# Kernel optimization log

Hardware: AMD Instinct MI355X
Metric: run time of the kernel (lower is better)

## Reference

```python
import jax, jax.numpy as jnp
import numpy as np

B, CIN, COUT, N, M, K = 8, 128, 256, 8192, 2048, 16
BN_EPS = 1e-5


def setup_inputs() -> dict:
    key = jax.random.key(0)
    k1, k2, k3 = jax.random.split(key, 3)
    x = jax.random.normal(k1, (B, CIN, N), dtype=jnp.float32)
    coords = jax.random.normal(k2, (B, 3, N), dtype=jnp.float32)
    W = jax.random.normal(k3, (COUT, CIN), dtype=jnp.float32) * 0.05  # 1x1 conv, bias=False
    gamma = jnp.ones((COUT,), dtype=jnp.float32)   # BatchNorm2d weight
    beta = jnp.zeros((COUT,), dtype=jnp.float32)   # BatchNorm2d bias
    return {"x": x, "coords": coords, "W": W, "gamma": gamma, "beta": beta}


def furthest_point_sampling(coords, num_samples):
    """coords: (B,3,N) -> indices (B,num_samples) int32. Greedy FPS starting at index 0."""
    pts = coords.transpose(0, 2, 1)  # (B,N,3)
    b, n, _ = pts.shape
    idx0 = jnp.zeros((b,), dtype=jnp.int32)
    mind0 = jnp.full((b, n), 1e10, dtype=pts.dtype)

    def step(carry, _):
        mind, last = carry
        lastpt = jnp.take_along_axis(pts, last[:, None, None], axis=1)  # (b,1,3)
        d = jnp.sum((pts - lastpt) ** 2, axis=-1)                        # (b,n)
        mind = jnp.minimum(mind, d)
        nxt = jnp.argmax(mind, axis=-1).astype(jnp.int32)
        return (mind, nxt), nxt

    (_, _), rest = jax.lax.scan(step, (mind0, idx0), None, length=num_samples - 1)
    return jnp.concatenate([idx0[:, None], rest.T], axis=1)  # (b,num_samples)


def reference(x, coords, W, gamma, beta):
    b = x.shape[0]
    fps_idx = furthest_point_sampling(coords, M)                # (B,M)
    pts = coords.transpose(0, 2, 1)                             # (B,N,3)
    bidx = jnp.arange(b)[:, None]
    fps_pts = pts[bidx, fps_idx]                                # (B,M,3)

    # squared-distance matrix via ||a||^2 + ||b||^2 - 2ab (avoids (B,M,N,3) temp)
    d = (jnp.sum(fps_pts ** 2, -1)[:, :, None]
         + jnp.sum(pts ** 2, -1)[:, None, :]
         - 2.0 * jnp.einsum('bmd,bnd->bmn', fps_pts, pts))      # (B,M,N)
    _, knn_idx = jax.lax.top_k(-d, K)                           # (B,M,K) nearest (sorted)

    x_t = x.transpose(0, 2, 1)                                  # (B,N,Cin)
    knn = x_t[jnp.arange(b)[:, None, None], knn_idx]            # (B,M,K,Cin)

    # PointwiseConv2D: 1x1 conv (no bias) + BatchNorm2d (batch stats) + ReLU
    h = jnp.einsum('bmkc,oc->bmko', knn, W)                     # (B,M,K,Cout)
    mean = jnp.mean(h, axis=(0, 1, 2))
    var = jnp.var(h, axis=(0, 1, 2))
    h = (h - mean) * jax.lax.rsqrt(var + BN_EPS) * gamma + beta
    h = jax.nn.relu(h)

    y = jnp.max(h, axis=2).transpose(0, 2, 1)                   # (B,Cout,M), max over k
    fps_coords = fps_pts.transpose(0, 2, 1)                     # (B,3,M)
    return y, fps_coords
```

## Files before the change

### kernel.cpp

```cpp
#include <hip/hip_runtime.h>
#include <math.h>

#define B_ 8
#define CIN_ 128
#define COUT_ 256
#define N_ 8192
#define M_ 2048
#define K_ 16

#define GEMM_BLOCKS 2048

__device__ __forceinline__ unsigned umax2(unsigned a, unsigned b) { return a > b ? a : b; }
__device__ __forceinline__ unsigned umin2(unsigned a, unsigned b) { return a < b ? a : b; }

__device__ __forceinline__ unsigned wave_reduce_umax(unsigned v) {
    v = umax2(v, (unsigned)__builtin_amdgcn_update_dpp(0, (int)v, 0x111, 0xf, 0xf, false));
    v = umax2(v, (unsigned)__builtin_amdgcn_update_dpp(0, (int)v, 0x112, 0xf, 0xf, false));
    v = umax2(v, (unsigned)__builtin_amdgcn_update_dpp(0, (int)v, 0x114, 0xf, 0xf, false));
    v = umax2(v, (unsigned)__builtin_amdgcn_update_dpp(0, (int)v, 0x118, 0xf, 0xf, false));
    v = umax2(v, (unsigned)__builtin_amdgcn_update_dpp(0, (int)v, 0x142, 0xf, 0xf, false));
    v = umax2(v, (unsigned)__builtin_amdgcn_update_dpp(0, (int)v, 0x143, 0xf, 0xf, false));
    return (unsigned)__builtin_amdgcn_readlane((int)v, 63);
}
__device__ __forceinline__ unsigned wave_reduce_umin(unsigned v) {
    v = umin2(v, (unsigned)__builtin_amdgcn_update_dpp(-1, (int)v, 0x111, 0xf, 0xf, false));
    v = umin2(v, (unsigned)__builtin_amdgcn_update_dpp(-1, (int)v, 0x112, 0xf, 0xf, false));
    v = umin2(v, (unsigned)__builtin_amdgcn_update_dpp(-1, (int)v, 0x114, 0xf, 0xf, false));
    v = umin2(v, (unsigned)__builtin_amdgcn_update_dpp(-1, (int)v, 0x118, 0xf, 0xf, false));
    v = umin2(v, (unsigned)__builtin_amdgcn_update_dpp(-1, (int)v, 0x142, 0xf, 0xf, false));
    v = umin2(v, (unsigned)__builtin_amdgcn_update_dpp(-1, (int)v, 0x143, 0xf, 0xf, false));
    return (unsigned)__builtin_amdgcn_readlane((int)v, 63);
}

__global__ __launch_bounds__(512) void fps_gemm_kernel(const float* __restrict__ coords,
                                                       const float* __restrict__ x,
                                                       const float* __restrict__ W,
                                                       float* __restrict__ fpts,
                                                       float* __restrict__ out_fps,
                                                       float* __restrict__ hp,
                                                       int* __restrict__ counts) {
    __shared__ union {
        struct {
            float4 pts[N_];
            unsigned long long kbuf[2][8];
            int wlist[M_];
        } f;
        struct {
            float Xs[64][128];
            float Wt[64][68];
        } g;
    } sm;

    const int tid = threadIdx.x;

    if (blockIdx.x < B_) {
#pragma clang fp contract(off)
        const int b = blockIdx.x;
        const int lane = tid & 63;
        const int wid = tid >> 6;
        const float* cb = coords + (size_t)b * 3 * N_;
        float4* pts = sm.f.pts;
        unsigned long long (*kbuf)[8] = sm.f.kbuf;
        int* wlist = sm.f.wlist;

        float px[16], py[16], pz[16], mind[16];
#pragma unroll
        for (int s = 0; s < 16; ++s) {
            int p = tid + s * 512;
            px[s] = cb[p];
            py[s] = cb[N_ + p];
            pz[s] = cb[2 * N_ + p];
            mind[s] = 1e10f;
            pts[p] = make_float4(px[s], py[s], pz[s], 0.f);
        }
        __syncthreads();
        float4 p0 = pts[0];
        float lx = p0.x, ly = p0.y, lz = p0.z;

        int par = 0;
        for (int m = 1; m < M_; ++m) {
            float bv = -1.0f; int bs = 0;
#pragma unroll
            for (int s = 0; s < 16; ++s) {
                float dx = px[s] - lx;
                float dy = py[s] - ly;
                float dz = pz[s] - lz;
                float d = __builtin_fmaf(dz, dz, __builtin_fmaf(dy, dy, dx * dx));
                float mn = fminf(mind[s], d);
                mind[s] = mn;
                if (mn > bv) { bv = mn; bs = s; }
            }
            int bi = tid + bs * 512;
            unsigned kd = __float_as_uint(bv);
            unsigned md = wave_reduce_umax(kd);
            unsigned cand = (kd == md) ? (unsigned)bi : 0xffffffffu;
            unsigned mi = wave_reduce_umin(cand);
            if (lane == 0)
                kbuf[par][wid] = ((unsigned long long)md << 32) |
                                 (unsigned long long)(0xffffffffu - mi);
            __syncthreads();
            const unsigned long long* kb = kbuf[par];
            ulonglong2 q0 = *(const ulonglong2*)&kb[0];
            ulonglong2 q1 = *(const ulonglong2*)&kb[2];
            ulonglong2 q2 = *(const ulonglong2*)&kb[4];
            ulonglong2 q3 = *(const ulonglong2*)&kb[6];
            unsigned long long a0 = q0.x > q0.y ? q0.x : q0.y;
            unsigned long long a1 = q1.x > q1.y ? q1.x : q1.y;
            unsigned long long a2 = q2.x > q2.y ? q2.x : q2.y;
            unsigned long long a3 = q3.x > q3.y ? q3.x : q3.y;
            unsigned long long b01 = a0 > a1 ? a0 : a1;
            unsigned long long b23 = a2 > a3 ? a2 : a3;
            unsigned long long best = b01 > b23 ? b01 : b23;
            int widx = (int)(0xffffffffu - (unsigned)(best & 0xffffffffull));
            widx = ((unsigned)widx < (unsigned)N_) ? widx : 0;
            float4 wp = pts[widx];
            lx = wp.x; ly = wp.y; lz = wp.z;
            if (tid == 0) wlist[m] = widx;
            par ^= 1;
        }

        __syncthreads();
        for (int mm = tid; mm < M_; mm += 512) {
            int wi = (mm == 0) ? 0 : wlist[mm];
            wi = ((unsigned)wi < (unsigned)N_) ? wi : 0;
            float4 wp = pts[wi];
            ((float4*)fpts)[b * M_ + mm] = make_float4(wp.x, wp.y, wp.z, 0.f);
            out_fps[(size_t)b * 3 * M_ + 0 * M_ + mm] = wp.x;
            out_fps[(size_t)b * 3 * M_ + 1 * M_ + mm] = wp.y;
            out_fps[(size_t)b * 3 * M_ + 2 * M_ + mm] = wp.z;
        }
    } else {
        const int gb = blockIdx.x - B_;
        if (tid < 32) counts[gb * 32 + tid] = 0;

        const int b = gb >> 8;
        const int rem = gb & 255;
        const int n0 = (rem >> 2) * 128;
        const int o0 = (rem & 3) * 64;
        const int tn = (tid & 31) * 4;
        const int to = (tid >> 5) * 4;
        const float* xg = x + (size_t)b * CIN_ * N_;
        float (*Xs)[128] = sm.g.Xs;
        float (*Wt)[68] = sm.g.Wt;

        float acc[4][4] = {};
        for (int kk = 0; kk < CIN_; kk += 64) {
#pragma unroll
            for (int i = 0; i < 16; ++i) {
                int e = tid + 512 * i;
                int r = e >> 7, q = e & 127;
                Xs[r][q] = xg[(size_t)(kk + r) * N_ + n0 + q];
            }
#pragma unroll
            for (int i = 0; i < 8; ++i) {
                int e = tid + 512 * i;
                int r = e >> 6, q = e & 63;
                Wt[q][r] = W[(size_t)(o0 + r) * CIN_ + kk + q];
            }
            __syncthreads();
#pragma unroll 8
            for (int c = 0; c < 64; ++c) {
                float4 a = *(const float4*)&Xs[c][tn];
                float4 bb = *(const float4*)&Wt[c][to];
                float av[4] = {a.x, a.y, a.z, a.w};
                float bv[4] = {bb.x, bb.y, bb.z, bb.w};
#pragma unroll
                for (int j = 0; j < 4; ++j)
#pragma unroll
                    for (int l = 0; l < 4; ++l)
                        acc[j][l] += av[j] * bv[l];
            }
            __syncthreads();
        }
#pragma unroll
        for (int j = 0; j < 4; ++j) {
            float4 v = make_float4(acc[j][0], acc[j][1], acc[j][2], acc[j][3]);
            *(float4*)&hp[((size_t)b * N_ + n0 + tn + j) * COUT_ + o0 + to] = v;
        }
    }
}

__global__ __launch_bounds__(256) void knn_kernel(const float* __restrict__ coords,
                                                  const float* __restrict__ fpts,
                                                  int* __restrict__ knn,
                                                  int* __restrict__ counts) {
#pragma clang fp contract(off)
    const int bidx = blockIdx.x;
    const int b = bidx >> 9;
    const int mg = bidx & 511;
    const int tid = threadIdx.x;
    const int lane = tid & 63;
    const int w = tid >> 6;
    const int m = mg * 4 + w;
    const int row = b * M_ + m;
    const float* cb = coords + (size_t)b * 3 * N_;

    __shared__ float4 tile[1024];

    float4 f = ((const float4*)fpts)[row];
    const float fx = f.x, fy = f.y, fz = f.z;
    const float sf = __builtin_fmaf(fz, fz, __builtin_fmaf(fy, fy, fx * fx));

    float ed = INFINITY; int ei = 0x7fffffff;
    float tau_d = INFINITY; int tau_i = 0x7fffffff;

    for (int t = 0; t < 8; ++t) {
        const int base = t * 1024;
#pragma unroll
        for (int j = 0; j < 4; ++j) {
            int idx = tid + 256 * j;
            int n = base + idx;
            float gx = cb[n], gy = cb[N_ + n], gz = cb[2 * N_ + n];
            float sp = __builtin_fmaf(gz, gz, __builtin_fmaf(gy, gy, gx * gx));
            tile[idx] = make_float4(gx, gy, gz, sp);
        }
        __syncthreads();
        for (int s = 0; s < 16; ++s) {
            int l = s * 64 + lane;
            float4 p = tile[l];
            int n = base + l;
            float dot = __builtin_fmaf(fz, p.z, __builtin_fmaf(fy, p.y, fx * p.x));
            float d = (sf + p.w) - 2.0f * dot;
            bool q = (d < tau_d) || (d == tau_d && n < tau_i);
            unsigned long long bal = __ballot(q);
            while (bal) {
                int lb = __ffsll(bal) - 1;
                bal &= bal - 1;
                float dv = __shfl(d, lb);
                int   iv = __shfl(n, lb);
                if ((dv < tau_d) || (dv == tau_d && iv < tau_i)) {
                    float pud = __shfl_up(ed, 1);
                    int   pui = __shfl_up(ei, 1);
                    bool cs = (dv < ed) || (dv == ed && iv < ei);
                    bool cp = (lane != 0) && ((dv < pud) || (dv == pud && iv < pui));
                    ed = cs ? (cp ? pud : dv) : ed;
                    ei = cs ? (cp ? pui : iv) : ei;
                    tau_d = __shfl(ed, 15);
                    tau_i = __shfl(ei, 15);
                }
            }
        }
        __syncthreads();
    }
    if (lane < K_) {
        int v = ei;
        v = ((unsigned)v < (unsigned)N_) ? v : 0;
        knn[(size_t)row * K_ + lane] = v;
        atomicAdd(&counts[b * N_ + v], 1);
    }
}

__global__ __launch_bounds__(256) void stats_partial_kernel(const float* __restrict__ hp,
                                                            const int* __restrict__ counts,
                                                            double* __restrict__ partial,
                                                            double* __restrict__ partial2) {
    const int o = threadIdx.x;
    const int base = blockIdx.x * 256;
    double s = 0.0, s2 = 0.0;
    for (int r = 0; r < 256; ++r) {
        int g = base + r;
        int cnt = counts[g];
        if (cnt) {
            double h = (double)hp[(size_t)g * COUT_ + o];
            double c = (double)cnt;
            double ch = c * h;
            s += ch;
            s2 += ch * h;
        }
    }
    partial[(size_t)blockIdx.x * 256 + o] = s;
    partial2[(size_t)blockIdx.x * 256 + o] = s2;
}

__global__ void bn_final_kernel(const double* __restrict__ partial,
                                const double* __restrict__ partial2,
                                const float* __restrict__ gamma,
                                const float* __restrict__ beta,
                                float* __restrict__ scale,
                                float* __restrict__ bias) {
    int o = threadIdx.x;
    double s = 0.0, s2 = 0.0;
    for (int j = 0; j < 256; ++j) {
        s += partial[(size_t)j * 256 + o];
        s2 += partial2[(size_t)j * 256 + o];
    }
    const double inv = 1.0 / (double)(B_ * M_ * K_);
    double mean = s * inv;
    double var = s2 * inv - mean * mean;
    if (var < 0.0) var = 0.0;
    double r = 1.0 / sqrt(var + 1e-5);
    double g = (double)gamma[o];
    scale[o] = (float)(r * g);
    bias[o] = (float)((double)beta[o] - mean * r * g);
}

__global__ __launch_bounds__(256) void finalize_kernel(const float* __restrict__ hp,
                                                       const int* __restrict__ knn,
                                                       const float* __restrict__ scale,
                                                       const float* __restrict__ bias,
                                                       float* __restrict__ y) {
    const int b = blockIdx.x >> 6;
    const int m0 = (blockIdx.x & 63) * 32;
    const int tid = threadIdx.x;
    __shared__ int kidx[512];
    __shared__ float tile[32][257];

    for (int e = tid; e < 512; e += 256) {
        int n = knn[(b * M_ + m0 + (e >> 4)) * K_ + (e & 15)];
        kidx[e] = ((unsigned)n < (unsigned)N_) ? n : 0;
    }
    __syncthreads();

    const float s = scale[tid];
    const float t = bias[tid];
    const float* hb = hp + (size_t)b * N_ * COUT_;
    for (int mm = 0; mm < 32; ++mm) {
        float v = -INFINITY;
#pragma unroll
        for (int k = 0; k < K_; ++k) {
            int n = kidx[mm * 16 + k];
            float h = hb[(size_t)n * COUT_ + tid];
            v = fmaxf(v, h * s + t);
        }
        v = fmaxf(v, 0.0f);
        tile[mm][tid] = v;
    }
    __syncthreads();
#pragma unroll
    for (int r = 0; r < 32; ++r) {
        int o2 = r * 8 + (tid >> 5);
        int mm = tid & 31;
        y[((size_t)b * COUT_ + o2) * M_ + m0 + mm] = tile[mm][o2];
    }
}

__global__ void sentinel_kernel(float* out, float v) { out[0] = v; }

extern "C" void kernel_launch(void* const* d_in, const int* in_sizes, int n_in,
                              void* d_out, int out_size, void* d_ws, size_t ws_size,
                              hipStream_t stream) {
    const float* x = (const float*)d_in[0];
    const float* coords = (const float*)d_in[1];
    const float* W = (const float*)d_in[2];
    const float* gamma = (const float*)d_in[3];
    const float* beta = (const float*)d_in[4];
    float* y = (float*)d_out;
    float* out_fps = y + (size_t)B_ * COUT_ * M_;

    if (n_in != 5 ||
        in_sizes[0] != B_ * CIN_ * N_ ||
        in_sizes[1] != B_ * 3 * N_ ||
        in_sizes[2] != COUT_ * CIN_ ||
        in_sizes[3] != COUT_ || in_sizes[4] != COUT_ ||
        out_size != B_ * COUT_ * M_ + B_ * 3 * M_) {
        sentinel_kernel<<<1, 1, 0, stream>>>(y, -2.0e6f);
        return;
    }

    const size_t HP_BYTES = (size_t)B_ * N_ * COUT_ * 4;
    const size_t FPTS_BYTES = (size_t)B_ * M_ * 16;
    const size_t KNN_BYTES = (size_t)B_ * M_ * K_ * 4;
    const size_t PART_BYTES = (size_t)256 * 256 * 8;
    const size_t CNT_BYTES = (size_t)B_ * N_ * 4;
    const size_t NEED = HP_BYTES + FPTS_BYTES + KNN_BYTES + 2 * PART_BYTES + CNT_BYTES + 8192;
    if (ws_size < NEED) {
        sentinel_kernel<<<1, 1, 0, stream>>>(y, -1.0e6f);
        return;
    }
    char* ws = (char*)d_ws;
    float* hp = (float*)ws;
    float* fpts = (float*)(ws + HP_BYTES);
    int* knn = (int*)(ws + HP_BYTES + FPTS_BYTES);
    double* partial = (double*)(ws + HP_BYTES + FPTS_BYTES + KNN_BYTES);
    double* partial2 = (double*)(ws + HP_BYTES + FPTS_BYTES + KNN_BYTES + PART_BYTES);
    int* counts = (int*)(ws + HP_BYTES + FPTS_BYTES + KNN_BYTES + 2 * PART_BYTES);
    float* scale = (float*)(ws + HP_BYTES + FPTS_BYTES + KNN_BYTES + 2 * PART_BYTES + CNT_BYTES);
    float* bias = scale + 256;

    fps_gemm_kernel<<<B_ + GEMM_BLOCKS, 512, 0, stream>>>(coords, x, W, fpts, out_fps, hp, counts);
    knn_kernel<<<B_ * 512, 256, 0, stream>>>(coords, fpts, knn, counts);
    stats_partial_kernel<<<256, 256, 0, stream>>>(hp, counts, partial, partial2);
    bn_final_kernel<<<1, 256, 0, stream>>>(partial, partial2, gamma, beta, scale, bias);
    finalize_kernel<<<512, 256, 0, stream>>>(hp, knn, scale, bias, y);
}
```

Baseline: 1.900 ms.

## Fuse FPS, GEMM and KNN into persistent kernel with per-sample flag streaming

Merges the KNN kernel into the FPS+GEMM launch as a persistent kernel with 240 worker blocks. The workers first loop over the GEMM tiles, then spin on per-sample atomic flags that the FPS blocks publish as each point is chosen, so KNN queries overlap with the serial FPS loop instead of waiting for it to finish. This removes the fpts buffer and a kernel launch, and adds two memsets. The risks are spin-wait overhead and a deadlock if not all blocks are co-resident, and the GEMM now runs on fewer blocks.

```diff
diff --git a/kernel.cpp b/kernel.cpp
--- a/kernel.cpp
+++ b/kernel.cpp
@@ -8,7 +8,9 @@
 #define M_ 2048
 #define K_ 16
 
-#define GEMM_BLOCKS 2048
+#define WORKERS 240
+#define NTILE 2048
+#define NGROUP 2048
 
 __device__ __forceinline__ unsigned umax2(unsigned a, unsigned b) { return a > b ? a : b; }
 __device__ __forceinline__ unsigned umin2(unsigned a, unsigned b) { return a < b ? a : b; }
@@ -32,13 +34,14 @@
     return (unsigned)__builtin_amdgcn_readlane((int)v, 63);
 }
 
-__global__ __launch_bounds__(512) void fps_gemm_kernel(const float* __restrict__ coords,
-                                                       const float* __restrict__ x,
-                                                       const float* __restrict__ W,
-                                                       float* __restrict__ fpts,
-                                                       float* __restrict__ out_fps,
-                                                       float* __restrict__ hp,
-                                                       int* __restrict__ counts) {
+__global__ __launch_bounds__(512) void mega_kernel(const float* __restrict__ coords,
+                                                   const float* __restrict__ x,
+                                                   const float* __restrict__ W,
+                                                   unsigned* __restrict__ wflag,
+                                                   float* __restrict__ out_fps,
+                                                   float* __restrict__ hp,
+                                                   int* __restrict__ knn,
+                                                   int* __restrict__ counts) {
     __shared__ union {
         struct {
             float4 pts[N_];
@@ -49,15 +52,18 @@
             float Xs[64][128];
             float Wt[64][68];
         } g;
+        struct {
+            float4 tile[1024];
+        } k;
     } sm;
 
     const int tid = threadIdx.x;
+    const int lane = tid & 63;
+    const int w = tid >> 6;
 
     if (blockIdx.x < B_) {
 #pragma clang fp contract(off)
         const int b = blockIdx.x;
-        const int lane = tid & 63;
-        const int wid = tid >> 6;
         const float* cb = coords + (size_t)b * 3 * N_;
         float4* pts = sm.f.pts;
         unsigned long long (*kbuf)[8] = sm.f.kbuf;
@@ -73,6 +79,9 @@
             mind[s] = 1e10f;
             pts[p] = make_float4(px[s], py[s], pz[s], 0.f);
         }
+        if (tid == 0)
+            __hip_atomic_store(&wflag[(size_t)b * M_], 0u,
+                               __ATOMIC_RELAXED, __HIP_MEMORY_SCOPE_AGENT);
         __syncthreads();
         float4 p0 = pts[0];
         float lx = p0.x, ly = p0.y, lz = p0.z;
@@ -96,8 +105,8 @@
             unsigned cand = (kd == md) ? (unsigned)bi : 0xffffffffu;
             unsigned mi = wave_reduce_umin(cand);
             if (lane == 0)
-                kbuf[par][wid] = ((unsigned long long)md << 32) |
-                                 (unsigned long long)(0xffffffffu - mi);
+                kbuf[par][w] = ((unsigned long long)md << 32) |
+                               (unsigned long long)(0xffffffffu - mi);
             __syncthreads();
             const unsigned long long* kb = kbuf[par];
             ulonglong2 q0 = *(const ulonglong2*)&kb[0];
@@ -115,7 +124,11 @@
             widx = ((unsigned)widx < (unsigned)N_) ? widx : 0;
             float4 wp = pts[widx];
             lx = wp.x; ly = wp.y; lz = wp.z;
-            if (tid == 0) wlist[m] = widx;
+            if (tid == 0) {
+                wlist[m] = widx;
+                __hip_atomic_store(&wflag[(size_t)b * M_ + m], (unsigned)widx,
+                                   __ATOMIC_RELAXED, __HIP_MEMORY_SCOPE_AGENT);
+            }
             par ^= 1;
         }
 
@@ -124,129 +137,130 @@
             int wi = (mm == 0) ? 0 : wlist[mm];
             wi = ((unsigned)wi < (unsigned)N_) ? wi : 0;
             float4 wp = pts[wi];
-            ((float4*)fpts)[b * M_ + mm] = make_float4(wp.x, wp.y, wp.z, 0.f);
             out_fps[(size_t)b * 3 * M_ + 0 * M_ + mm] = wp.x;
             out_fps[(size_t)b * 3 * M_ + 1 * M_ + mm] = wp.y;
             out_fps[(size_t)b * 3 * M_ + 2 * M_ + mm] = wp.z;
         }
     } else {
-        const int gb = blockIdx.x - B_;
-        if (tid < 32) counts[gb * 32 + tid] = 0;
-
-        const int b = gb >> 8;
-        const int rem = gb & 255;
-        const int n0 = (rem >> 2) * 128;
-        const int o0 = (rem & 3) * 64;
-        const int tn = (tid & 31) * 4;
-        const int to = (tid >> 5) * 4;
-        const float* xg = x + (size_t)b * CIN_ * N_;
+        const int wkr = blockIdx.x - B_;
+
         float (*Xs)[128] = sm.g.Xs;
         float (*Wt)[68] = sm.g.Wt;
-
-        float acc[4][4] = {};
-        for (int kk = 0; kk < CIN_; kk += 64) {
-#pragma unroll
-            for (int i = 0; i < 16; ++i) {
-                int e = tid + 512 * i;
-                int r = e >> 7, q = e & 127;
-                Xs[r][q] = xg[(size_t)(kk + r) * N_ + n0 + q];
+        for (int t = wkr; t < NTILE; t += WORKERS) {
+            const int b = t >> 8;
+            const int rem = t & 255;
+            const int n0 = (rem >> 2) * 128;
+            const int o0 = (rem & 3) * 64;
+            const int tn = (tid & 31) * 4;
+            const int to = (tid >> 5) * 4;
+            const float* xg = x + (size_t)b * CIN_ * N_;
+
+            float acc[4][4] = {};
+            for (int kk = 0; kk < CIN_; kk += 64) {
+#pragma unroll
+                for (int i = 0; i < 16; ++i) {
+                    int e = tid + 512 * i;
+                    int r = e >> 7, q = e & 127;
+                    Xs[r][q] = xg[(size_t)(kk + r) * N_ + n0 + q];
+                }
+#pragma unroll
+                for (int i = 0; i < 8; ++i) {
+                    int e = tid + 512 * i;
+                    int r = e >> 6, q = e & 63;
+                    Wt[q][r] = W[(size_t)(o0 + r) * CIN_ + kk + q];
+                }
+                __syncthreads();
+#pragma unroll 8
+                for (int c = 0; c < 64; ++c) {
+                    float4 a = *(const float4*)&Xs[c][tn];
+                    float4 bb = *(const float4*)&Wt[c][to];
+                    float av[4] = {a.x, a.y, a.z, a.w};
+                    float bv[4] = {bb.x, bb.y, bb.z, bb.w};
+#pragma unroll
+                    for (int j = 0; j < 4; ++j)
+#pragma unroll
+                        for (int l = 0; l < 4; ++l)
+                            acc[j][l] += av[j] * bv[l];
+                }
+                __syncthreads();
             }
 #pragma unroll
-            for (int i = 0; i < 8; ++i) {
-                int e = tid + 512 * i;
-                int r = e >> 6, q = e & 63;
-                Wt[q][r] = W[(size_t)(o0 + r) * CIN_ + kk + q];
+            for (int j = 0; j < 4; ++j) {
+                float4 v = make_float4(acc[j][0], acc[j][1], acc[j][2], acc[j][3]);
+                *(float4*)&hp[((size_t)b * N_ + n0 + tn + j) * COUT_ + o0 + to] = v;
             }
-            __syncthreads();
-#pragma unroll 8
-            for (int c = 0; c < 64; ++c) {
-                float4 a = *(const float4*)&Xs[c][tn];
-                float4 bb = *(const float4*)&Wt[c][to];
-                float av[4] = {a.x, a.y, a.z, a.w};
-                float bv[4] = {bb.x, bb.y, bb.z, bb.w};
-#pragma unroll
-                for (int j = 0; j < 4; ++j)
-#pragma unroll
-                    for (int l = 0; l < 4; ++l)
-                        acc[j][l] += av[j] * bv[l];
-            }
-            __syncthreads();
-        }
-#pragma unroll
-        for (int j = 0; j < 4; ++j) {
-            float4 v = make_float4(acc[j][0], acc[j][1], acc[j][2], acc[j][3]);
-            *(float4*)&hp[((size_t)b * N_ + n0 + tn + j) * COUT_ + o0 + to] = v;
-        }
-    }
-}
-
-__global__ __launch_bounds__(256) void knn_kernel(const float* __restrict__ coords,
-                                                  const float* __restrict__ fpts,
-                                                  int* __restrict__ knn,
-                                                  int* __restrict__ counts) {
+        }
+
+        {
 #pragma clang fp contract(off)
-    const int bidx = blockIdx.x;
-    const int b = bidx >> 9;
-    const int mg = bidx & 511;
-    const int tid = threadIdx.x;
-    const int lane = tid & 63;
-    const int w = tid >> 6;
-    const int m = mg * 4 + w;
-    const int row = b * M_ + m;
-    const float* cb = coords + (size_t)b * 3 * N_;
-
-    __shared__ float4 tile[1024];
-
-    float4 f = ((const float4*)fpts)[row];
-    const float fx = f.x, fy = f.y, fz = f.z;
-    const float sf = __builtin_fmaf(fz, fz, __builtin_fmaf(fy, fy, fx * fx));
-
-    float ed = INFINITY; int ei = 0x7fffffff;
-    float tau_d = INFINITY; int tau_i = 0x7fffffff;
-
-    for (int t = 0; t < 8; ++t) {
-        const int base = t * 1024;
-#pragma unroll
-        for (int j = 0; j < 4; ++j) {
-            int idx = tid + 256 * j;
-            int n = base + idx;
-            float gx = cb[n], gy = cb[N_ + n], gz = cb[2 * N_ + n];
-            float sp = __builtin_fmaf(gz, gz, __builtin_fmaf(gy, gy, gx * gx));
-            tile[idx] = make_float4(gx, gy, gz, sp);
-        }
-        __syncthreads();
-        for (int s = 0; s < 16; ++s) {
-            int l = s * 64 + lane;
-            float4 p = tile[l];
-            int n = base + l;
-            float dot = __builtin_fmaf(fz, p.z, __builtin_fmaf(fy, p.y, fx * p.x));
-            float d = (sf + p.w) - 2.0f * dot;
-            bool q = (d < tau_d) || (d == tau_d && n < tau_i);
-            unsigned long long bal = __ballot(q);
-            while (bal) {
-                int lb = __ffsll(bal) - 1;
-                bal &= bal - 1;
-                float dv = __shfl(d, lb);
-                int   iv = __shfl(n, lb);
-                if ((dv < tau_d) || (dv == tau_d && iv < tau_i)) {
-                    float pud = __shfl_up(ed, 1);
-                    int   pui = __shfl_up(ei, 1);
-                    bool cs = (dv < ed) || (dv == ed && iv < ei);
-                    bool cp = (lane != 0) && ((dv < pud) || (dv == pud && iv < pui));
-                    ed = cs ? (cp ? pud : dv) : ed;
-                    ei = cs ? (cp ? pui : iv) : ei;
-                    tau_d = __shfl(ed, 15);
-                    tau_i = __shfl(ei, 15);
+            float4* tile = sm.k.tile;
+            for (int g = wkr; g < NGROUP; g += WORKERS) {
+                const int b = g & 7;
+                const int mg = g >> 3;
+                const int m = mg * 8 + w;
+                const int row = b * M_ + m;
+                const float* cb = coords + (size_t)b * 3 * N_;
+
+                unsigned widx;
+                while ((widx = __hip_atomic_load(&wflag[row], __ATOMIC_RELAXED,
+                                                 __HIP_MEMORY_SCOPE_AGENT)) == 0xffffffffu)
+                    __builtin_amdgcn_s_sleep(2);
+                widx = (widx < (unsigned)N_) ? widx : 0;
+
+                const float fx = cb[widx];
+                const float fy = cb[N_ + widx];
+                const float fz = cb[2 * N_ + widx];
+                const float sf = __builtin_fmaf(fz, fz, __builtin_fmaf(fy, fy, fx * fx));
+
+                float ed = INFINITY; int ei = 0x7fffffff;
+                float tau_d = INFINITY; int tau_i = 0x7fffffff;
+
+                for (int t = 0; t < 8; ++t) {
+                    const int base = t * 1024;
+#pragma unroll
+                    for (int j = 0; j < 2; ++j) {
+                        int idx = tid + 512 * j;
+                        int n = base + idx;
+                        float gx = cb[n], gy = cb[N_ + n], gz = cb[2 * N_ + n];
+                        float sp = __builtin_fmaf(gz, gz, __builtin_fmaf(gy, gy, gx * gx));
+                        tile[idx] = make_float4(gx, gy, gz, sp);
+                    }
+                    __syncthreads();
+                    for (int s = 0; s < 16; ++s) {
+                        int l = s * 64 + lane;
+                        float4 p = tile[l];
+                        int n = base + l;
+                        float dot = __builtin_fmaf(fz, p.z, __builtin_fmaf(fy, p.y, fx * p.x));
+                        float d = (sf + p.w) - 2.0f * dot;
+                        bool q = (d < tau_d) || (d == tau_d && n < tau_i);
+                        unsigned long long bal = __ballot(q);
+                        while (bal) {
+                            int lb = __ffsll(bal) - 1;
+                            bal &= bal - 1;
+                            float dv = __shfl(d, lb);
+                            int   iv = __shfl(n, lb);
+                            if ((dv < tau_d) || (dv == tau_d && iv < tau_i)) {
+                                float pud = __shfl_up(ed, 1);
+                                int   pui = __shfl_up(ei, 1);
+                                bool cs = (dv < ed) || (dv == ed && iv < ei);
+                                bool cp = (lane != 0) && ((dv < pud) || (dv == pud && iv < pui));
+                                ed = cs ? (cp ? pud : dv) : ed;
+                                ei = cs ? (cp ? pui : iv) : ei;
+                                tau_d = __shfl(ed, 15);
+                                tau_i = __shfl(ei, 15);
+                            }
+                        }
+                    }
+                    __syncthreads();
+                }
+                if (lane < K_) {
+                    int v = ei;
+                    v = ((unsigned)v < (unsigned)N_) ? v : 0;
+                    knn[(size_t)row * K_ + lane] = v;
+                    atomicAdd(&counts[b * N_ + v], 1);
                 }
             }
         }
-        __syncthreads();
-    }
-    if (lane < K_) {
-        int v = ei;
-        v = ((unsigned)v < (unsigned)N_) ? v : 0;
-        knn[(size_t)row * K_ + lane] = v;
-        atomicAdd(&counts[b * N_ + v], 1);
     }
 }
 
@@ -358,27 +372,30 @@
     }
 
     const size_t HP_BYTES = (size_t)B_ * N_ * COUT_ * 4;
-    const size_t FPTS_BYTES = (size_t)B_ * M_ * 16;
     const size_t KNN_BYTES = (size_t)B_ * M_ * K_ * 4;
     const size_t PART_BYTES = (size_t)256 * 256 * 8;
     const size_t CNT_BYTES = (size_t)B_ * N_ * 4;
-    const size_t NEED = HP_BYTES + FPTS_BYTES + KNN_BYTES + 2 * PART_BYTES + CNT_BYTES + 8192;
+    const size_t WFLAG_BYTES = (size_t)B_ * M_ * 4;
+    const size_t NEED = HP_BYTES + KNN_BYTES + 2 * PART_BYTES + CNT_BYTES + WFLAG_BYTES + 8192;
     if (ws_size < NEED) {
         sentinel_kernel<<<1, 1, 0, stream>>>(y, -1.0e6f);
         return;
     }
     char* ws = (char*)d_ws;
     float* hp = (float*)ws;
-    float* fpts = (float*)(ws + HP_BYTES);
-    int* knn = (int*)(ws + HP_BYTES + FPTS_BYTES);
-    double* partial = (double*)(ws + HP_BYTES + FPTS_BYTES + KNN_BYTES);
-    double* partial2 = (double*)(ws + HP_BYTES + FPTS_BYTES + KNN_BYTES + PART_BYTES);
-    int* counts = (int*)(ws + HP_BYTES + FPTS_BYTES + KNN_BYTES + 2 * PART_BYTES);
-    float* scale = (float*)(ws + HP_BYTES + FPTS_BYTES + KNN_BYTES + 2 * PART_BYTES + CNT_BYTES);
+    int* knn = (int*)(ws + HP_BYTES);
+    double* partial = (double*)(ws + HP_BYTES + KNN_BYTES);
+    double* partial2 = (double*)(ws + HP_BYTES + KNN_BYTES + PART_BYTES);
+    int* counts = (int*)(ws + HP_BYTES + KNN_BYTES + 2 * PART_BYTES);
+    unsigned* wflag = (unsigned*)(ws + HP_BYTES + KNN_BYTES + 2 * PART_BYTES + CNT_BYTES);
+    float* scale = (float*)(ws + HP_BYTES + KNN_BYTES + 2 * PART_BYTES + CNT_BYTES + WFLAG_BYTES);
     float* bias = scale + 256;
 
-    fps_gemm_kernel<<<B_ + GEMM_BLOCKS, 512, 0, stream>>>(coords, x, W, fpts, out_fps, hp, counts);
-    knn_kernel<<<B_ * 512, 256, 0, stream>>>(coords, fpts, knn, counts);
+    (void)hipMemsetAsync(counts, 0, CNT_BYTES, stream);
+    (void)hipMemsetAsync(wflag, 0xFF, WFLAG_BYTES, stream);
+
+    mega_kernel<<<B_ + WORKERS, 512, 0, stream>>>(coords, x, W, wflag, out_fps,
+                                                  hp, knn, counts);
     stats_partial_kernel<<<256, 256, 0, stream>>>(hp, counts, partial, partial2);
     bn_final_kernel<<<1, 256, 0, stream>>>(partial, partial2, gamma, beta, scale, bias);
     finalize_kernel<<<512, 256, 0, stream>>>(hp, knn, scale, bias, y);
```

Result: faster. 1.763 ms (-7.2%).
